# Optimization experiments

Hardware: AMD Instinct MI355X
Metric: run time of the kernel (lower is better)

Reference implementation:

```python
import jax, jax.numpy as jnp
import numpy as np

N = 50000        # nodes
E = 800000       # edges (before self loops)
IN = 128         # in_channels
HID = 32         # hidden_channels (per head)
HEADS = 4
OUT = 10         # out_channels (classes)
G = 64           # graphs in batch
NEG_SLOPE = 0.2  # PyG GATConv default leaky relu slope


def setup_inputs() -> dict:
    key = jax.random.key(0)
    ks = jax.random.split(key, 12)
    s = 0.05
    return {
        "x": jax.random.normal(ks[0], (N, IN), jnp.float32),
        "W1": jax.random.normal(ks[1], (IN, HEADS * HID), jnp.float32) * s,
        "a1_src": jax.random.normal(ks[2], (HEADS, HID), jnp.float32) * s,
        "a1_dst": jax.random.normal(ks[3], (HEADS, HID), jnp.float32) * s,
        "b1": jnp.zeros((HEADS * HID,), jnp.float32),
        "W2": jax.random.normal(ks[4], (HEADS * HID, HEADS * HID), jnp.float32) * s,
        "a2_src": jax.random.normal(ks[5], (HEADS, HID), jnp.float32) * s,
        "a2_dst": jax.random.normal(ks[6], (HEADS, HID), jnp.float32) * s,
        "b2": jnp.zeros((HEADS * HID,), jnp.float32),
        "Wl": jax.random.normal(ks[7], (HEADS * HID, OUT), jnp.float32) * s,
        "bl": jnp.zeros((OUT,), jnp.float32),
        "edge_index": jax.random.randint(ks[8], (2, E), 0, N, jnp.int32),
        "batch": jnp.sort(jax.random.randint(ks[9], (N,), 0, G, jnp.int32)),
    }


def gat_conv(x, src, dst, W, a_src, a_dst, b):
    """PyG GATConv (concat=True, self loops already in src/dst). Eval mode: no dropout."""
    n = x.shape[0]
    h = (x @ W).reshape(n, HEADS, HID)                       # [N,H,C]
    al_s = jnp.einsum('nhc,hc->nh', h, a_src)                # [N,H]
    al_d = jnp.einsum('nhc,hc->nh', h, a_dst)
    e = jax.nn.leaky_relu(al_s[src] + al_d[dst], NEG_SLOPE)  # [Etot,H]
    # segment softmax over destination node neighborhoods
    m = jax.ops.segment_max(e, dst, num_segments=n)
    m = jnp.where(jnp.isfinite(m), m, 0.0)
    p = jnp.exp(e - m[dst])
    z = jax.ops.segment_sum(p, dst, num_segments=n)
    alpha = p / (z[dst] + 1e-16)                             # [Etot,H]
    out = jax.ops.segment_sum(h[src] * alpha[:, :, None], dst, num_segments=n)
    return out.reshape(n, HEADS * HID) + b


def reference(x, W1, a1_src, a1_dst, b1, W2, a2_src, a2_dst, b2, Wl, bl,
              edge_index, batch):
    n = x.shape[0]
    loops = jnp.arange(n, dtype=edge_index.dtype)
    src = jnp.concatenate([edge_index[0], loops])
    dst = jnp.concatenate([edge_index[1], loops])

    h = jax.nn.elu(gat_conv(x, src, dst, W1, a1_src, a1_dst, b1))
    h = gat_conv(h, src, dst, W2, a2_src, a2_dst, b2)

    # global_mean_pool over graph ids
    counts = jax.ops.segment_sum(jnp.ones((n,), h.dtype), batch, num_segments=G)
    pooled = jax.ops.segment_sum(h, batch, num_segments=G) / jnp.maximum(counts, 1.0)[:, None]

    logits = pooled @ Wl + bl
    return jax.nn.softmax(logits, axis=1)
```

## Files before the change

### kernel.cpp

```cpp
#include <hip/hip_runtime.h>
#include <hip/hip_bf16.h>
#include <math.h>

#define HEADS 4
#define HID 32
#define FDIM 128
#define OUTC 10
#define NEG 0.2f
#define ECAP 512
#define BCAP 5440

typedef __attribute__((ext_vector_type(4))) float f32x4;
typedef __attribute__((ext_vector_type(8))) short bf16x8;

static __device__ __forceinline__ float lrelu(float v) { return v > 0.f ? v : NEG * v; }

static __device__ __forceinline__ unsigned bfr(float f) {
  unsigned u = __float_as_uint(f);
  return (u + 0x7fffu + ((u >> 16) & 1u)) >> 16;
}
static __device__ __forceinline__ float blo(unsigned u) { return __uint_as_float(u << 16); }
static __device__ __forceinline__ float bhi(unsigned u) { return __uint_as_float(u & 0xffff0000u); }

#define CHUNK 4096

__global__ __launch_bounds__(256) void k_bin(
    const int* __restrict__ ei, int* __restrict__ gbcur,
    int2* __restrict__ bbuf, int E, int n) {
  __shared__ int h[256];
  __shared__ int cur[256];
  int tid = threadIdx.x;
  h[tid] = 0;
  __syncthreads();
  int base = blockIdx.x * CHUNK;
  int tot = E + n;
  #pragma unroll
  for (int r = 0; r < 16; ++r) {
    int e = base + r * 256 + tid;
    if (e < tot) {
      int dst = (e < E) ? ei[E + e] : (e - E);
      atomicAdd(&h[dst >> 8], 1);
    }
  }
  __syncthreads();
  if (h[tid]) cur[tid] = tid * BCAP + atomicAdd(&gbcur[tid], h[tid]);
  __syncthreads();
  #pragma unroll
  for (int r = 0; r < 16; ++r) {
    int e = base + r * 256 + tid;
    if (e < tot) {
      int src = (e < E) ? ei[e] : (e - E);
      int dst = (e < E) ? ei[E + e] : (e - E);
      int pos = atomicAdd(&cur[dst >> 8], 1);
      bbuf[pos] = make_int2(src, dst);
    }
  }
}

__global__ __launch_bounds__(256) void k_build(
    const int2* __restrict__ bbuf, const int* __restrict__ gbcur,
    int* __restrict__ offs, int* __restrict__ csr, int* __restrict__ dpos,
    int n) {
  __shared__ int deg[256];
  __shared__ int sc[256];
  __shared__ int cur[256];
  int b = blockIdx.x;
  int tid = threadIdx.x;
  int ebeg = b * BCAP;
  int eend = ebeg + gbcur[b];
  deg[tid] = 0;
  __syncthreads();
  for (int i = ebeg + tid; i < eend; i += 256)
    atomicAdd(&deg[bbuf[i].y & 255], 1);
  __syncthreads();
  int v = deg[tid];
  sc[tid] = v;
  __syncthreads();
  #pragma unroll
  for (int off = 1; off < 256; off <<= 1) {
    int t = (tid >= off) ? sc[tid - off] : 0;
    __syncthreads();
    sc[tid] += t;
    __syncthreads();
  }
  int excl = sc[tid] - v;
  int dst0 = b * 256 + tid;
  if (dst0 < n) offs[dst0] = ebeg + excl;
  cur[tid] = ebeg + excl;
  __syncthreads();
  for (int i = ebeg + tid; i < eend; i += 256) {
    int2 sd = bbuf[i];
    int pos = atomicAdd(&cur[sd.y & 255], 1);
    csr[pos] = sd.x;
    dpos[pos] = sd.y;
  }
}

__global__ __launch_bounds__(256) void k_prep(
    const float* __restrict__ W1, const float* __restrict__ W2,
    const float* __restrict__ a1s, const float* __restrict__ a1d,
    const float* __restrict__ a2s, const float* __restrict__ a2d,
    uint4* __restrict__ WF) {
  int layer = blockIdx.y;
  const float* W = layer ? W2 : W1;
  __shared__ float wa[128][8];
  int tid = threadIdx.x;
  #pragma unroll
  for (int q = 0; q < 4; ++q) {
    int e = tid * 4 + q;
    int k = e >> 3, c = e & 7;
    int h = c & 3;
    const float* av = (c < 4 ? (layer ? a2s : a1s) : (layer ? a2d : a1d)) + h * 32;
    const float* wr = W + (size_t)k * 128 + h * 32;
    float s = 0.f;
    #pragma unroll
    for (int j = 0; j < 32; j += 4) {
      float4 wv = *reinterpret_cast<const float4*>(wr + j);
      float4 a4 = *reinterpret_cast<const float4*>(av + j);
      s += wv.x * a4.x + wv.y * a4.y + wv.z * a4.z + wv.w * a4.w;
    }
    wa[k][c] = s;
  }
  __syncthreads();
  int gid = blockIdx.x * 256 + tid;
  if (gid >= 2304) return;
  int lane = gid & 63, frag = gid >> 6;
  int t = frag / 9, ct = frag - t * 9;
  int quad = lane >> 4, r = lane & 15;
  int kbase = t * 32 + quad * 8;
  unsigned v[8];
  if (ct < 8) {
    int col = ct * 16 + r;
    #pragma unroll
    for (int j = 0; j < 8; ++j) v[j] = bfr(W[(size_t)(kbase + j) * 128 + col]);
  } else if (r < 8) {
    #pragma unroll
    for (int j = 0; j < 8; ++j) v[j] = bfr(wa[kbase + j][r]);
  } else {
    #pragma unroll
    for (int j = 0; j < 8; ++j) v[j] = 0;
  }
  uint4 pk;
  pk.x = v[0] | (v[1] << 16);
  pk.y = v[2] | (v[3] << 16);
  pk.z = v[4] | (v[5] << 16);
  pk.w = v[6] | (v[7] << 16);
  WF[layer * 2304 + gid] = pk;
}

template<bool BF16IN>
__global__ __launch_bounds__(256) void k_mm(
    const void* __restrict__ Xv, const uint4* __restrict__ WF,
    unsigned short* __restrict__ H, float* __restrict__ AL, int n) {
  __shared__ uint4 wf[2304];
  int tid = threadIdx.x;
  #pragma unroll
  for (int i = 0; i < 9; ++i) wf[i * 256 + tid] = WF[i * 256 + tid];
  __syncthreads();
  int lane = tid & 63, wid = tid >> 6;
  int quad = lane >> 4, r = lane & 15;
  int rowbase = blockIdx.x * 64 + wid * 16;
  int arow = rowbase + r;
  int arowc = arow < n ? arow : 0;
  const bf16x8* wfs = (const bf16x8*)wf;

  f32x4 acc[9];
  #pragma unroll
  for (int ct = 0; ct < 9; ++ct) acc[ct] = 0;

  #pragma unroll
  for (int t = 0; t < 4; ++t) {
    bf16x8 a;
    if (BF16IN) {
      const uint4* xp = reinterpret_cast<const uint4*>(Xv) + (size_t)arowc * 16;
      uint4 u = xp[t * 4 + quad];
      a = *reinterpret_cast<const bf16x8*>(&u);
    } else {
      const float* xp = reinterpret_cast<const float*>(Xv) + (size_t)arowc * 128 + quad * 8;
      float4 x0 = *reinterpret_cast<const float4*>(xp + t * 32);
      float4 x1 = *reinterpret_cast<const float4*>(xp + t * 32 + 4);
      a[0] = (short)bfr(x0.x); a[1] = (short)bfr(x0.y);
      a[2] = (short)bfr(x0.z); a[3] = (short)bfr(x0.w);
      a[4] = (short)bfr(x1.x); a[5] = (short)bfr(x1.y);
      a[6] = (short)bfr(x1.z); a[7] = (short)bfr(x1.w);
    }
    #pragma unroll
    for (int ct = 0; ct < 9; ++ct)
      acc[ct] = __builtin_amdgcn_mfma_f32_16x16x32_bf16(
          a, wfs[(t * 9 + ct) * 64 + lane], acc[ct], 0, 0, 0);
  }

  int orow0 = rowbase + quad * 4;
  #pragma unroll
  for (int rr = 0; rr < 4; ++rr) {
    int orow = orow0 + rr;
    if (orow < n) {
      unsigned short* hp = H + (size_t)orow * 128 + r;
      #pragma unroll
      for (int ct = 0; ct < 8; ++ct) hp[ct * 16] = (unsigned short)bfr(acc[ct][rr]);
      if (r < 8) AL[(size_t)orow * 8 + r] = acc[8][rr];
    }
  }
}

template<bool ELU_OUT, bool POOL>
__global__ __launch_bounds__(256) void k_agg(
    const unsigned short* __restrict__ H, const float* __restrict__ AL,
    const int* __restrict__ offs, const int* __restrict__ csr,
    const int* __restrict__ dpos, const int* __restrict__ gbcur,
    const float* __restrict__ bias, unsigned short* __restrict__ OUT,
    const int* __restrict__ batch, float* __restrict__ pooled,
    int* __restrict__ gcnt, int n) {
  __shared__ __align__(16) char smem[ECAP * 4 + ECAP * 16];
  int* s_l = (int*)smem;
  float (*p_l)[4] = (float(*)[4])(smem + ECAP * 4);
  float (*o_l)[132] = (float(*)[132])smem;
  __shared__ int g_l[16];
  int tid = threadIdx.x;
  int lane = tid & 63;
  int r = lane & 15;
  int gg = (tid >> 6) * 4 + (lane >> 4);
  int nbase = blockIdx.x * 16;
  int node = nbase + gg;
  bool nvalid = node < n;
  int nodec = nvalid ? node : 0;
  int bkt = nbase >> 8;
  int bend = bkt * BCAP + gbcur[bkt];
  int beg = offs[nodec];
  int nxt = nodec + 1;
  int end = nvalid ? ((nxt >= n || (nxt & 255) == 0) ? bend : offs[nxt]) : beg;
  int ebeg = offs[nbase];
  int nend = nbase + 16;
  int eend = (nend >= n || (nend & 255) == 0) ? bend : offs[nend];
  int hsel = r >> 2;
  const uint4* hb = reinterpret_cast<const uint4*>(H) + r;

  if (POOL && r == 0) g_l[gg] = nvalid ? batch[node] : -1;

  float z = 0.f;
  float acc[8];
  #pragma unroll
  for (int k = 0; k < 8; ++k) acc[k] = 0.f;

  for (int c0 = ebeg; c0 < eend; c0 += ECAP) {
    int clen = min(ECAP, eend - c0);
    __syncthreads();
    for (int i = tid; i < clen; i += 256) {
      int s = csr[c0 + i];
      int d = dpos[c0 + i];
      float4 as_ = *reinterpret_cast<const float4*>(AL + (size_t)s * 8);
      float4 ad = *reinterpret_cast<const float4*>(AL + (size_t)d * 8 + 4);
      s_l[i] = s;
      float4 p;
      p.x = __expf(lrelu(as_.x + ad.x));
      p.y = __expf(lrelu(as_.y + ad.y));
      p.z = __expf(lrelu(as_.z + ad.z));
      p.w = __expf(lrelu(as_.w + ad.w));
      *reinterpret_cast<float4*>(&p_l[i][0]) = p;
    }
    __syncthreads();
    int lo = max(beg, c0), hi = min(end, c0 + clen);
    int cnt = hi - lo;
    int lbase = lo - c0;
    for (int j0 = 0; j0 < cnt; j0 += 4) {
      int j1 = j0 + 1, j2 = j0 + 2, j3 = j0 + 3;
      bool v1 = j1 < cnt, v2 = j2 < cnt, v3 = j3 < cnt;
      int jB = lbase + (v1 ? j1 : j0);
      int jC = lbase + (v2 ? j2 : j0);
      int jD = lbase + (v3 ? j3 : j0);
      int jA = lbase + j0;
      int sA = s_l[jA], sB = s_l[jB], sC = s_l[jC], sD = s_l[jD];
      float pA = p_l[jA][hsel];
      float pB = v1 ? p_l[jB][hsel] : 0.f;
      float pC = v2 ? p_l[jC][hsel] : 0.f;
      float pD = v3 ? p_l[jD][hsel] : 0.f;
      z += (pA + pB) + (pC + pD);
      uint4 uA = hb[(size_t)sA * 16];
      uint4 uB = hb[(size_t)sB * 16];
      uint4 uC = hb[(size_t)sC * 16];
      uint4 uD = hb[(size_t)sD * 16];
      acc[0] = fmaf(pA, blo(uA.x), acc[0]); acc[1] = fmaf(pA, bhi(uA.x), acc[1]);
      acc[2] = fmaf(pA, blo(uA.y), acc[2]); acc[3] = fmaf(pA, bhi(uA.y), acc[3]);
      acc[4] = fmaf(pA, blo(uA.z), acc[4]); acc[5] = fmaf(pA, bhi(uA.z), acc[5]);
      acc[6] = fmaf(pA, blo(uA.w), acc[6]); acc[7] = fmaf(pA, bhi(uA.w), acc[7]);
      acc[0] = fmaf(pB, blo(uB.x), acc[0]); acc[1] = fmaf(pB, bhi(uB.x), acc[1]);
      acc[2] = fmaf(pB, blo(uB.y), acc[2]); acc[3] = fmaf(pB, bhi(uB.y), acc[3]);
      acc[4] = fmaf(pB, blo(uB.z), acc[4]); acc[5] = fmaf(pB, bhi(uB.z), acc[5]);
      acc[6] = fmaf(pB, blo(uB.w), acc[6]); acc[7] = fmaf(pB, bhi(uB.w), acc[7]);
      acc[0] = fmaf(pC, blo(uC.x), acc[0]); acc[1] = fmaf(pC, bhi(uC.x), acc[1]);
      acc[2] = fmaf(pC, blo(uC.y), acc[2]); acc[3] = fmaf(pC, bhi(uC.y), acc[3]);
      acc[4] = fmaf(pC, blo(uC.z), acc[4]); acc[5] = fmaf(pC, bhi(uC.z), acc[5]);
      acc[6] = fmaf(pC, blo(uC.w), acc[6]); acc[7] = fmaf(pC, bhi(uC.w), acc[7]);
      acc[0] = fmaf(pD, blo(uD.x), acc[0]); acc[1] = fmaf(pD, bhi(uD.x), acc[1]);
      acc[2] = fmaf(pD, blo(uD.y), acc[2]); acc[3] = fmaf(pD, bhi(uD.y), acc[3]);
      acc[4] = fmaf(pD, blo(uD.z), acc[4]); acc[5] = fmaf(pD, bhi(uD.z), acc[5]);
      acc[6] = fmaf(pD, blo(uD.w), acc[6]); acc[7] = fmaf(pD, bhi(uD.w), acc[7]);
    }
  }

  float inv = 1.f / (z + 1e-16f);
  int f0 = r * 8;
  float4 b0 = *reinterpret_cast<const float4*>(bias + f0);
  float4 b1 = *reinterpret_cast<const float4*>(bias + f0 + 4);
  float o[8];
  o[0] = acc[0] * inv + b0.x; o[1] = acc[1] * inv + b0.y;
  o[2] = acc[2] * inv + b0.z; o[3] = acc[3] * inv + b0.w;
  o[4] = acc[4] * inv + b1.x; o[5] = acc[5] * inv + b1.y;
  o[6] = acc[6] * inv + b1.z; o[7] = acc[7] * inv + b1.w;
  if (ELU_OUT) {
    #pragma unroll
    for (int k = 0; k < 8; ++k) o[k] = o[k] > 0.f ? o[k] : expm1f(o[k]);
  }

  if (!POOL) {
    if (nvalid) {
      uint4 pk;
      pk.x = bfr(o[0]) | (bfr(o[1]) << 16);
      pk.y = bfr(o[2]) | (bfr(o[3]) << 16);
      pk.z = bfr(o[4]) | (bfr(o[5]) << 16);
      pk.w = bfr(o[6]) | (bfr(o[7]) << 16);
      reinterpret_cast<uint4*>(OUT)[(size_t)node * 16 + r] = pk;
    }
  } else {
    __syncthreads();
    *reinterpret_cast<float4*>(&o_l[gg][f0]) = make_float4(o[0], o[1], o[2], o[3]);
    *reinterpret_cast<float4*>(&o_l[gg][f0 + 4]) = make_float4(o[4], o[5], o[6], o[7]);
    __syncthreads();
    if (tid < 128) {
      int f = tid;
      float accp = 0.f; int cur = -1;
      #pragma unroll
      for (int i = 0; i < 16; ++i) {
        int g = g_l[i];
        if (g != cur) {
          if (cur >= 0) atomicAdd(&pooled[(size_t)cur * 128 + f], accp);
          cur = g; accp = 0.f;
        }
        if (g >= 0) accp += o_l[i][f];
      }
      if (cur >= 0) atomicAdd(&pooled[(size_t)cur * 128 + f], accp);
    } else if (tid == 128) {
      int cur = -1, c = 0;
      #pragma unroll
      for (int i = 0; i < 16; ++i) {
        int g = g_l[i];
        if (g != cur) { if (cur >= 0) atomicAdd(&gcnt[cur], c); cur = g; c = 0; }
        if (g >= 0) ++c;
      }
      if (cur >= 0) atomicAdd(&gcnt[cur], c);
    }
  }
}

__global__ void k_head(const float* __restrict__ pooled, const int* __restrict__ gcnt,
                       const float* __restrict__ Wl, const float* __restrict__ bl,
                       float* __restrict__ out) {
  int g = blockIdx.x;
  int lane = threadIdx.x;
  float cnt = fmaxf((float)gcnt[g], 1.f);
  float pA = pooled[(size_t)g * 128 + lane] / cnt;
  float pB = pooled[(size_t)g * 128 + lane + 64] / cnt;
  float l[OUTC];
  #pragma unroll
  for (int o = 0; o < OUTC; ++o) {
    float s = pA * Wl[lane * OUTC + o] + pB * Wl[(lane + 64) * OUTC + o];
    #pragma unroll
    for (int off = 32; off; off >>= 1) s += __shfl_xor(s, off);
    l[o] = s + bl[o];
  }
  float mx = l[0];
  #pragma unroll
  for (int o = 1; o < OUTC; ++o) mx = fmaxf(mx, l[o]);
  float se = 0.f;
  #pragma unroll
  for (int o = 0; o < OUTC; ++o) { l[o] = __expf(l[o] - mx); se += l[o]; }
  if (lane == 0) {
    float inv = 1.f / se;
    #pragma unroll
    for (int o = 0; o < OUTC; ++o) out[g * OUTC + o] = l[o] * inv;
  }
}

extern "C" void kernel_launch(void* const* d_in, const int* in_sizes, int n_in,
                              void* d_out, int out_size, void* d_ws, size_t ws_size,
                              hipStream_t stream) {
  const float* x   = (const float*)d_in[0];
  const float* W1  = (const float*)d_in[1];
  const float* a1s = (const float*)d_in[2];
  const float* a1d = (const float*)d_in[3];
  const float* b1  = (const float*)d_in[4];
  const float* W2  = (const float*)d_in[5];
  const float* a2s = (const float*)d_in[6];
  const float* a2d = (const float*)d_in[7];
  const float* b2  = (const float*)d_in[8];
  const float* Wl  = (const float*)d_in[9];
  const float* bl  = (const float*)d_in[10];
  const int* ei    = (const int*)d_in[11];
  const int* batch = (const int*)d_in[12];
  const int N = in_sizes[12];
  const int E = in_sizes[11] / 2;
  const int G = out_size / OUTC;
  float* out = (float*)d_out;
  (void)n_in; (void)ws_size;

  const int tot = E + N;
  const int NB = (N + 255) / 256;

  char* w = (char*)d_ws;
  auto alloc = [&](size_t bytes) { char* p = w; w += (bytes + 255) & ~(size_t)255; return (void*)p; };
  unsigned short* H = (unsigned short*)alloc((size_t)N * FDIM * sizeof(unsigned short));
  unsigned short* ACT = (unsigned short*)alloc((size_t)N * FDIM * sizeof(unsigned short));
  float* AL     = (float*)alloc((size_t)N * 8 * sizeof(float));
  uint4* WF     = (uint4*)alloc(2 * 2304 * sizeof(uint4));
  int*   offs   = (int*)alloc((size_t)N * sizeof(int));
  int*   csr    = (int*)alloc((size_t)NB * BCAP * sizeof(int));
  int*   dpos   = (int*)alloc((size_t)NB * BCAP * sizeof(int));
  int2*  bbuf   = (int2*)alloc((size_t)NB * BCAP * sizeof(int2));
  char* z0 = w;
  int*   gbcur  = (int*)alloc(256 * sizeof(int));
  int*   gcnt   = (int*)alloc((size_t)G * sizeof(int));
  float* pooled = (float*)alloc((size_t)G * FDIM * sizeof(float));
  size_t zbytes = (size_t)(w - z0);
  hipMemsetAsync(z0, 0, zbytes, stream);

  int ab4 = (tot + CHUNK - 1) / CHUNK;
  k_bin<<<ab4, 256, 0, stream>>>(ei, gbcur, bbuf, E, N);
  k_build<<<NB, 256, 0, stream>>>(bbuf, gbcur, offs, csr, dpos, N);

  k_prep<<<dim3(9, 2), 256, 0, stream>>>(W1, W2, a1s, a1d, a2s, a2d, WF);

  int gb = (N + 63) / 64;
  int ab = (N + 15) / 16;
  k_mm<false><<<gb, 256, 0, stream>>>(x, WF, H, AL, N);
  k_agg<true, false><<<ab, 256, 0, stream>>>(H, AL, offs, csr, dpos, gbcur, b1, ACT, batch, pooled, gcnt, N);
  k_mm<true><<<gb, 256, 0, stream>>>(ACT, WF + 2304, H, AL, N);
  k_agg<false, true><<<ab, 256, 0, stream>>>(H, AL, offs, csr, dpos, gbcur, b2, nullptr, batch, pooled, gcnt, N);

  k_head<<<G, 64, 0, stream>>>(pooled, gcnt, Wl, bl, out);
}
```

Before: 229.8 us.

## Assign one wavefront per node in aggregation and pack CSR src/dst pairs

The aggregation kernel now maps one 64-lane wavefront per destination node instead of a 16-lane group, splitting the edge loop across four lane quarters and combining partial sums with cross-lane shuffles. Blocks cover 4 nodes instead of 16, and the shared edge staging buffer shrinks. The CSR source and destination arrays are merged into one int2 array, so each edge needs a single coalesced load. This is meant to shorten the per-node serial gather chain and raise memory-level parallelism on the H row gathers. In exchange there are four times more blocks, the shuffle reduction adds work, and only a quarter of the lanes are active in the epilogue.

```diff
diff --git a/kernel.cpp b/kernel.cpp
--- a/kernel.cpp
+++ b/kernel.cpp
@@ -7,7 +7,7 @@
 #define FDIM 128
 #define OUTC 10
 #define NEG 0.2f
-#define ECAP 512
+#define ECAP 192
 #define BCAP 5440
 
 typedef __attribute__((ext_vector_type(4))) float f32x4;
@@ -59,8 +59,7 @@
 
 __global__ __launch_bounds__(256) void k_build(
     const int2* __restrict__ bbuf, const int* __restrict__ gbcur,
-    int* __restrict__ offs, int* __restrict__ csr, int* __restrict__ dpos,
-    int n) {
+    int* __restrict__ offs, int2* __restrict__ cd, int n) {
   __shared__ int deg[256];
   __shared__ int sc[256];
   __shared__ int cur[256];
@@ -91,8 +90,7 @@
   for (int i = ebeg + tid; i < eend; i += 256) {
     int2 sd = bbuf[i];
     int pos = atomicAdd(&cur[sd.y & 255], 1);
-    csr[pos] = sd.x;
-    dpos[pos] = sd.y;
+    cd[pos] = sd;
   }
 }
 
@@ -206,8 +204,8 @@
 template<bool ELU_OUT, bool POOL>
 __global__ __launch_bounds__(256) void k_agg(
     const unsigned short* __restrict__ H, const float* __restrict__ AL,
-    const int* __restrict__ offs, const int* __restrict__ csr,
-    const int* __restrict__ dpos, const int* __restrict__ gbcur,
+    const int* __restrict__ offs, const int2* __restrict__ cd,
+    const int* __restrict__ gbcur,
     const float* __restrict__ bias, unsigned short* __restrict__ OUT,
     const int* __restrict__ batch, float* __restrict__ pooled,
     int* __restrict__ gcnt, int n) {
@@ -215,13 +213,15 @@
   int* s_l = (int*)smem;
   float (*p_l)[4] = (float(*)[4])(smem + ECAP * 4);
   float (*o_l)[132] = (float(*)[132])smem;
-  __shared__ int g_l[16];
+  __shared__ int g_l[4];
   int tid = threadIdx.x;
   int lane = tid & 63;
-  int r = lane & 15;
-  int gg = (tid >> 6) * 4 + (lane >> 4);
-  int nbase = blockIdx.x * 16;
-  int node = nbase + gg;
+  int wid = tid >> 6;
+  int fl = lane & 15;
+  int qw = lane >> 4;
+  int hsel = fl >> 2;
+  int nbase = blockIdx.x * 4;
+  int node = nbase + wid;
   bool nvalid = node < n;
   int nodec = nvalid ? node : 0;
   int bkt = nbase >> 8;
@@ -230,12 +230,11 @@
   int nxt = nodec + 1;
   int end = nvalid ? ((nxt >= n || (nxt & 255) == 0) ? bend : offs[nxt]) : beg;
   int ebeg = offs[nbase];
-  int nend = nbase + 16;
+  int nend = nbase + 4;
   int eend = (nend >= n || (nend & 255) == 0) ? bend : offs[nend];
-  int hsel = r >> 2;
-  const uint4* hb = reinterpret_cast<const uint4*>(H) + r;
-
-  if (POOL && r == 0) g_l[gg] = nvalid ? batch[node] : -1;
+  const uint4* hb = reinterpret_cast<const uint4*>(H) + fl;
+
+  if (POOL && lane == 0) g_l[wid] = nvalid ? batch[node] : -1;
 
   float z = 0.f;
   float acc[8];
@@ -246,11 +245,10 @@
     int clen = min(ECAP, eend - c0);
     __syncthreads();
     for (int i = tid; i < clen; i += 256) {
-      int s = csr[c0 + i];
-      int d = dpos[c0 + i];
-      float4 as_ = *reinterpret_cast<const float4*>(AL + (size_t)s * 8);
-      float4 ad = *reinterpret_cast<const float4*>(AL + (size_t)d * 8 + 4);
-      s_l[i] = s;
+      int2 sd = cd[c0 + i];
+      float4 as_ = *reinterpret_cast<const float4*>(AL + (size_t)sd.x * 8);
+      float4 ad = *reinterpret_cast<const float4*>(AL + (size_t)sd.y * 8 + 4);
+      s_l[i] = sd.x;
       float4 p;
       p.x = __expf(lrelu(as_.x + ad.x));
       p.y = __expf(lrelu(as_.y + ad.y));
@@ -261,24 +259,18 @@
     __syncthreads();
     int lo = max(beg, c0), hi = min(end, c0 + clen);
     int cnt = hi - lo;
-    int lbase = lo - c0;
-    for (int j0 = 0; j0 < cnt; j0 += 4) {
-      int j1 = j0 + 1, j2 = j0 + 2, j3 = j0 + 3;
-      bool v1 = j1 < cnt, v2 = j2 < cnt, v3 = j3 < cnt;
-      int jB = lbase + (v1 ? j1 : j0);
-      int jC = lbase + (v2 ? j2 : j0);
-      int jD = lbase + (v3 ? j3 : j0);
-      int jA = lbase + j0;
-      int sA = s_l[jA], sB = s_l[jB], sC = s_l[jC], sD = s_l[jD];
-      float pA = p_l[jA][hsel];
-      float pB = v1 ? p_l[jB][hsel] : 0.f;
-      float pC = v2 ? p_l[jC][hsel] : 0.f;
-      float pD = v3 ? p_l[jD][hsel] : 0.f;
-      z += (pA + pB) + (pC + pD);
+    int lb = lo - c0;
+    for (int j0 = 0; j0 < cnt; j0 += 8) {
+      int jA = j0 + qw, jB = jA + 4;
+      bool vA = jA < cnt, vB = jB < cnt;
+      int iA = lb + (vA ? jA : 0);
+      int iB = lb + (vB ? jB : 0);
+      int sA = s_l[iA], sB = s_l[iB];
+      float pA = vA ? p_l[iA][hsel] : 0.f;
+      float pB = vB ? p_l[iB][hsel] : 0.f;
+      z += pA + pB;
       uint4 uA = hb[(size_t)sA * 16];
       uint4 uB = hb[(size_t)sB * 16];
-      uint4 uC = hb[(size_t)sC * 16];
-      uint4 uD = hb[(size_t)sD * 16];
       acc[0] = fmaf(pA, blo(uA.x), acc[0]); acc[1] = fmaf(pA, bhi(uA.x), acc[1]);
       acc[2] = fmaf(pA, blo(uA.y), acc[2]); acc[3] = fmaf(pA, bhi(uA.y), acc[3]);
       acc[4] = fmaf(pA, blo(uA.z), acc[4]); acc[5] = fmaf(pA, bhi(uA.z), acc[5]);
@@ -287,50 +279,54 @@
       acc[2] = fmaf(pB, blo(uB.y), acc[2]); acc[3] = fmaf(pB, bhi(uB.y), acc[3]);
       acc[4] = fmaf(pB, blo(uB.z), acc[4]); acc[5] = fmaf(pB, bhi(uB.z), acc[5]);
       acc[6] = fmaf(pB, blo(uB.w), acc[6]); acc[7] = fmaf(pB, bhi(uB.w), acc[7]);
-      acc[0] = fmaf(pC, blo(uC.x), acc[0]); acc[1] = fmaf(pC, bhi(uC.x), acc[1]);
-      acc[2] = fmaf(pC, blo(uC.y), acc[2]); acc[3] = fmaf(pC, bhi(uC.y), acc[3]);
-      acc[4] = fmaf(pC, blo(uC.z), acc[4]); acc[5] = fmaf(pC, bhi(uC.z), acc[5]);
-      acc[6] = fmaf(pC, blo(uC.w), acc[6]); acc[7] = fmaf(pC, bhi(uC.w), acc[7]);
-      acc[0] = fmaf(pD, blo(uD.x), acc[0]); acc[1] = fmaf(pD, bhi(uD.x), acc[1]);
-      acc[2] = fmaf(pD, blo(uD.y), acc[2]); acc[3] = fmaf(pD, bhi(uD.y), acc[3]);
-      acc[4] = fmaf(pD, blo(uD.z), acc[4]); acc[5] = fmaf(pD, bhi(uD.z), acc[5]);
-      acc[6] = fmaf(pD, blo(uD.w), acc[6]); acc[7] = fmaf(pD, bhi(uD.w), acc[7]);
-    }
+    }
+  }
+
+  z += __shfl_xor(z, 16);
+  z += __shfl_xor(z, 32);
+  #pragma unroll
+  for (int k = 0; k < 8; ++k) {
+    acc[k] += __shfl_xor(acc[k], 16);
+    acc[k] += __shfl_xor(acc[k], 32);
   }
 
   float inv = 1.f / (z + 1e-16f);
-  int f0 = r * 8;
-  float4 b0 = *reinterpret_cast<const float4*>(bias + f0);
-  float4 b1 = *reinterpret_cast<const float4*>(bias + f0 + 4);
+  int f0 = fl * 8;
   float o[8];
-  o[0] = acc[0] * inv + b0.x; o[1] = acc[1] * inv + b0.y;
-  o[2] = acc[2] * inv + b0.z; o[3] = acc[3] * inv + b0.w;
-  o[4] = acc[4] * inv + b1.x; o[5] = acc[5] * inv + b1.y;
-  o[6] = acc[6] * inv + b1.z; o[7] = acc[7] * inv + b1.w;
-  if (ELU_OUT) {
-    #pragma unroll
-    for (int k = 0; k < 8; ++k) o[k] = o[k] > 0.f ? o[k] : expm1f(o[k]);
+  if (lane < 16) {
+    float4 b0 = *reinterpret_cast<const float4*>(bias + f0);
+    float4 b1 = *reinterpret_cast<const float4*>(bias + f0 + 4);
+    o[0] = acc[0] * inv + b0.x; o[1] = acc[1] * inv + b0.y;
+    o[2] = acc[2] * inv + b0.z; o[3] = acc[3] * inv + b0.w;
+    o[4] = acc[4] * inv + b1.x; o[5] = acc[5] * inv + b1.y;
+    o[6] = acc[6] * inv + b1.z; o[7] = acc[7] * inv + b1.w;
+    if (ELU_OUT) {
+      #pragma unroll
+      for (int k = 0; k < 8; ++k) o[k] = o[k] > 0.f ? o[k] : expm1f(o[k]);
+    }
   }
 
   if (!POOL) {
-    if (nvalid) {
+    if (lane < 16 && nvalid) {
       uint4 pk;
       pk.x = bfr(o[0]) | (bfr(o[1]) << 16);
       pk.y = bfr(o[2]) | (bfr(o[3]) << 16);
       pk.z = bfr(o[4]) | (bfr(o[5]) << 16);
       pk.w = bfr(o[6]) | (bfr(o[7]) << 16);
-      reinterpret_cast<uint4*>(OUT)[(size_t)node * 16 + r] = pk;
+      reinterpret_cast<uint4*>(OUT)[(size_t)node * 16 + fl] = pk;
     }
   } else {
     __syncthreads();
-    *reinterpret_cast<float4*>(&o_l[gg][f0]) = make_float4(o[0], o[1], o[2], o[3]);
-    *reinterpret_cast<float4*>(&o_l[gg][f0 + 4]) = make_float4(o[4], o[5], o[6], o[7]);
+    if (lane < 16) {
+      *reinterpret_cast<float4*>(&o_l[wid][f0]) = make_float4(o[0], o[1], o[2], o[3]);
+      *reinterpret_cast<float4*>(&o_l[wid][f0 + 4]) = make_float4(o[4], o[5], o[6], o[7]);
+    }
     __syncthreads();
     if (tid < 128) {
       int f = tid;
       float accp = 0.f; int cur = -1;
       #pragma unroll
-      for (int i = 0; i < 16; ++i) {
+      for (int i = 0; i < 4; ++i) {
         int g = g_l[i];
         if (g != cur) {
           if (cur >= 0) atomicAdd(&pooled[(size_t)cur * 128 + f], accp);
@@ -342,7 +338,7 @@
     } else if (tid == 128) {
       int cur = -1, c = 0;
       #pragma unroll
-      for (int i = 0; i < 16; ++i) {
+      for (int i = 0; i < 4; ++i) {
         int g = g_l[i];
         if (g != cur) { if (cur >= 0) atomicAdd(&gcnt[cur], c); cur = g; c = 0; }
         if (g >= 0) ++c;
@@ -413,8 +409,7 @@
   float* AL     = (float*)alloc((size_t)N * 8 * sizeof(float));
   uint4* WF     = (uint4*)alloc(2 * 2304 * sizeof(uint4));
   int*   offs   = (int*)alloc((size_t)N * sizeof(int));
-  int*   csr    = (int*)alloc((size_t)NB * BCAP * sizeof(int));
-  int*   dpos   = (int*)alloc((size_t)NB * BCAP * sizeof(int));
+  int2*  cd     = (int2*)alloc((size_t)NB * BCAP * sizeof(int2));
   int2*  bbuf   = (int2*)alloc((size_t)NB * BCAP * sizeof(int2));
   char* z0 = w;
   int*   gbcur  = (int*)alloc(256 * sizeof(int));
@@ -425,16 +420,16 @@
 
   int ab4 = (tot + CHUNK - 1) / CHUNK;
   k_bin<<<ab4, 256, 0, stream>>>(ei, gbcur, bbuf, E, N);
-  k_build<<<NB, 256, 0, stream>>>(bbuf, gbcur, offs, csr, dpos, N);
+  k_build<<<NB, 256, 0, stream>>>(bbuf, gbcur, offs, cd, N);
 
   k_prep<<<dim3(9, 2), 256, 0, stream>>>(W1, W2, a1s, a1d, a2s, a2d, WF);
 
   int gb = (N + 63) / 64;
-  int ab = (N + 15) / 16;
+  int ab = (N + 3) / 4;
   k_mm<false><<<gb, 256, 0, stream>>>(x, WF, H, AL, N);
-  k_agg<true, false><<<ab, 256, 0, stream>>>(H, AL, offs, csr, dpos, gbcur, b1, ACT, batch, pooled, gcnt, N);
+  k_agg<true, false><<<ab, 256, 0, stream>>>(H, AL, offs, cd, gbcur, b1, ACT, batch, pooled, gcnt, N);
   k_mm<true><<<gb, 256, 0, stream>>>(ACT, WF + 2304, H, AL, N);
-  k_agg<false, true><<<ab, 256, 0, stream>>>(H, AL, offs, csr, dpos, gbcur, b2, nullptr, batch, pooled, gcnt, N);
+  k_agg<false, true><<<ab, 256, 0, stream>>>(H, AL, offs, cd, gbcur, b2, nullptr, batch, pooled, gcnt, N);
 
   k_head<<<G, 64, 0, stream>>>(pooled, gcnt, Wl, bl, out);
 }
```

After: 303.1 us. 31.9% more time.
